# Kernel optimization log

Hardware: AMD Instinct MI355X
Metric: run time of the kernel (lower is better)

## Reference

```python
import jax, jax.numpy as jnp
import numpy as np

N = 16384
K = 16

def _w(k, shape):
    return jax.random.normal(k, shape, jnp.float32) * 0.05

def setup_inputs() -> dict:
    key = jax.random.key(0)
    ks = jax.random.split(key, 20)
    return {
        "img_feat": jax.random.normal(ks[0], (1, 32, N), jnp.float32),
        "cloud": jax.random.uniform(ks[1], (1, N, 3), jnp.float32),
        "conv1_w": _w(ks[2], (64, 32)),   "conv1_b": _w(ks[3], (64,)),
        "conv2_w": _w(ks[4], (128, 64)),  "conv2_b": _w(ks[5], (128,)),
        "psconv1_w": _w(ks[6], (256, 128)), "psconv1_b": _w(ks[7], (256,)),
        "psconv2_w": _w(ks[8], (128, 256)), "psconv2_b": _w(ks[9], (128,)),
        "pconv1_w": _w(ks[10], (64, 3)),  "pconv1_b": _w(ks[11], (64,)),
        "pconv2_w": _w(ks[12], (128, 64)),"pconv2_b": _w(ks[13], (128,)),
        "final_w": _w(ks[14], (32, 416)), "final_b": _w(ks[15], (32,)),
        "topk": K,
    }

def reference(img_feat, cloud, conv1_w, conv1_b, conv2_w, conv2_b,
              psconv1_w, psconv1_b, psconv2_w, psconv2_b,
              pconv1_w, pconv1_b, pconv2_w, pconv2_b,
              final_w, final_b, topk):
    lrelu = lambda x: jax.nn.leaky_relu(x, 0.01)
    pts = cloud[0]            # [N,3]  (module assumes bs=1)
    imf = img_feat[0].T       # [N,32]
    # point MLP: pconv1 -> lrelu -> pconv2 (Conv1d kernel=1 == per-point linear)
    cf = lrelu(pts @ pconv1_w.T + pconv1_b) @ pconv2_w.T + pconv2_b  # [N,128]
    # KNN: k smallest euclidean distances (self included)
    sq = jnp.sum(pts * pts, axis=-1)                 # [N]
    d2 = sq[:, None] + sq[None, :] - 2.0 * (pts @ pts.T)  # [N,N]
    _, idx = jax.lax.top_k(-d2, topk)                # [N,K]
    nb_pts = pts[idx]                                # [N,K,3]
    dist = jnp.sqrt(jnp.maximum(jnp.sum((pts[:, None, :] - nb_pts) ** 2, -1), 1e-12))
    wgt = jax.nn.softmax(-dist, axis=1)              # [N,K]
    nb_img = imf[idx]                                # [N,K,32]
    nb_cf = cf[idx]                                  # [N,K,128]
    sf = lrelu(nb_img @ conv1_w.T + conv1_b) @ conv2_w.T + conv2_b         # [N,K,128]
    sfp = lrelu(nb_cf @ psconv1_w.T + psconv1_b) @ psconv2_w.T + psconv2_b # [N,K,128]
    sf = jnp.max(sf * wgt[:, :, None], axis=1)       # weighted max-pool -> [N,128]
    sfp = jnp.max(sfp * wgt[:, :, None], axis=1)     # [N,128]
    final = jnp.concatenate([sfp, imf, sf, cf], axis=1)  # [N,416]
    out = lrelu(final) @ final_w.T + final_b         # [N,32]
    return out.T[None]                               # [1,32,N]
```

## Files before the change

kernel.cpp:

```cpp
#include <hip/hip_runtime.h>
#include <math.h>

#define N 16384
#define KNN 16
#define G 16
#define NCELL 4096

typedef __attribute__((ext_vector_type(8))) short bf16x8;
typedef __attribute__((ext_vector_type(4))) float f32x4;
typedef unsigned short ushort_t;
typedef unsigned long long u64;

__device__ __forceinline__ float lrelu(float a) { return a > 0.f ? a : 0.01f * a; }

__device__ __forceinline__ ushort_t f2bf(float f) {
  unsigned u = __float_as_uint(f);
  u += 0x7FFF + ((u >> 16) & 1);
  return (ushort_t)(u >> 16);
}
__device__ __forceinline__ float bf2f(ushort_t h) {
  return __uint_as_float((unsigned)h << 16);
}
__device__ __forceinline__ int lanerank(u64 mask) {
  return __builtin_amdgcn_mbcnt_hi((unsigned)(mask >> 32),
         __builtin_amdgcn_mbcnt_lo((unsigned)mask, 0));
}
__device__ __forceinline__ int cellof(float x) {
  int c = (int)(x * (float)G);
  return c < 0 ? 0 : (c > G - 1 ? G - 1 : c);
}

#define PPB 64
__global__ __launch_bounds__(256) void prepw_kernel(
    const float* __restrict__ img, const float* __restrict__ cloud,
    const float* __restrict__ p1w, const float* __restrict__ p1b,
    const float* __restrict__ p2w, const float* __restrict__ p2b,
    const float* __restrict__ ps1w, const float* __restrict__ ps2w,
    const float* __restrict__ c1w, const float* __restrict__ c2w,
    const float* __restrict__ fw,
    float4* __restrict__ pts4, ushort_t* __restrict__ cfh,
    ushort_t* __restrict__ imfh,
    ushort_t* __restrict__ w1h, ushort_t* __restrict__ w2h,
    ushort_t* __restrict__ c1h, ushort_t* __restrict__ c2h,
    float* __restrict__ fwp2, int* __restrict__ count) {
  int t = threadIdx.x;
  if (blockIdx.x >= 256) {
    int e = (blockIdx.x - 256) * 256 + t;
    if (e < 32768) w1h[e] = f2bf(ps1w[e]);
    else if (e < 65536) w2h[e - 32768] = f2bf(ps2w[e - 32768]);
    else if (e < 67584) c1h[e - 65536] = f2bf(c1w[e - 65536]);
    else if (e < 75776) c2h[e - 67584] = f2bf(c2w[e - 67584]);
    else if (e < 89088) {
      int e2 = e - 75776;
      int j4 = e2 >> 7, r2 = e2 & 127;
      int ch = r2 >> 2, sub = r2 & 3;
      fwp2[e2] = fw[ch * 416 + j4 * 4 + sub];
    }
    return;
  }
  __shared__ alignas(16) float w2t[64 * 132];
  __shared__ alignas(16) float hs[PPB * 68];
  __shared__ alignas(16) float w1s[192];
  __shared__ alignas(16) float b1s[64];
  __shared__ alignas(16) float b2s[128];
  __shared__ float ptmp[PPB * 3];
  __shared__ float psx[PPB], psy[PPB], psz[PPB];
  int pb = blockIdx.x * PPB;

  for (int e = t; e < 128 * 64; e += 256) {
    int ch = e >> 6, k = e & 63;
    w2t[k * 132 + ch] = p2w[e];
  }
  if (t < 192) w1s[t] = p1w[t];
  if (t < 64) b1s[t] = p1b[t];
  if (t < 128) b2s[t] = p2b[t];
  if (t < PPB * 3) ptmp[t] = cloud[pb * 3 + t];
  __syncthreads();
  if (t < PPB) {
    float x = ptmp[t * 3], y = ptmp[t * 3 + 1], z = ptmp[t * 3 + 2];
    psx[t] = x; psy[t] = y; psz[t] = z;
    pts4[pb + t] = make_float4(x, y, z, x * x + y * y + z * z);
    int cid = ((cellof(z) << 4) | cellof(y)) << 4 | cellof(x);
    atomicAdd(&count[cid], 1);
  }
  for (int e = t; e < 32 * PPB; e += 256) {
    int c = e >> 6, p = e & 63;
    imfh[(size_t)(pb + p) * 32 + c] = f2bf(img[(size_t)c * N + pb + p]);
  }
  __syncthreads();
  for (int e = t; e < PPB * 64; e += 256) {
    int pt_ = e >> 6, ch = e & 63;
    float a = b1s[ch] + psx[pt_] * w1s[ch * 3] + psy[pt_] * w1s[ch * 3 + 1] +
              psz[pt_] * w1s[ch * 3 + 2];
    hs[pt_ * 68 + ch] = lrelu(a);
  }
  __syncthreads();
  for (int e = t; e < PPB * 32; e += 256) {
    int pt_ = e >> 5, c4 = (e & 31) << 2;
    float4 acc = *(const float4*)&b2s[c4];
    const float* hrow = &hs[pt_ * 68];
    #pragma unroll
    for (int k = 0; k < 64; k += 4) {
      float4 h4 = *(const float4*)&hrow[k];
      float4 w0 = *(const float4*)&w2t[(k + 0) * 132 + c4];
      float4 w1_ = *(const float4*)&w2t[(k + 1) * 132 + c4];
      float4 w2_ = *(const float4*)&w2t[(k + 2) * 132 + c4];
      float4 w3 = *(const float4*)&w2t[(k + 3) * 132 + c4];
      acc.x = fmaf(h4.x, w0.x, fmaf(h4.y, w1_.x, fmaf(h4.z, w2_.x, fmaf(h4.w, w3.x, acc.x))));
      acc.y = fmaf(h4.x, w0.y, fmaf(h4.y, w1_.y, fmaf(h4.z, w2_.y, fmaf(h4.w, w3.y, acc.y))));
      acc.z = fmaf(h4.x, w0.z, fmaf(h4.y, w1_.z, fmaf(h4.z, w2_.z, fmaf(h4.w, w3.z, acc.z))));
      acc.w = fmaf(h4.x, w0.w, fmaf(h4.y, w1_.w, fmaf(h4.z, w2_.w, fmaf(h4.w, w3.w, acc.w))));
    }
    unsigned lo = (unsigned)f2bf(acc.x) | ((unsigned)f2bf(acc.y) << 16);
    unsigned hi = (unsigned)f2bf(acc.z) | ((unsigned)f2bf(acc.w) << 16);
    *(uint2*)&cfh[(size_t)(pb + pt_) * 128 + c4] = make_uint2(lo, hi);
  }
}

__global__ __launch_bounds__(256) void scan_kernel(
    const int* __restrict__ count, int* __restrict__ cellStart,
    int* __restrict__ cellofs) {
  __shared__ int part[256];
  int t = threadIdx.x;
  int local[16];
  int s = 0;
  #pragma unroll
  for (int j = 0; j < 16; ++j) { local[j] = s; s += count[t * 16 + j]; }
  part[t] = s;
  __syncthreads();
  for (int off = 1; off < 256; off <<= 1) {
    int v = (t >= off) ? part[t - off] : 0;
    __syncthreads();
    part[t] += v;
    __syncthreads();
  }
  int base = part[t] - s;
  #pragma unroll
  for (int j = 0; j < 16; ++j) {
    int v = base + local[j];
    cellStart[t * 16 + j] = v;
    cellofs[t * 16 + j] = v;
  }
  if (t == 255) cellStart[NCELL] = part[255];
}

__global__ __launch_bounds__(256) void scatter_kernel(
    const float4* __restrict__ pts4, const ushort_t* __restrict__ cfh,
    const ushort_t* __restrict__ imfh, int* __restrict__ cellofs,
    float4* __restrict__ spts, ushort_t* __restrict__ cfs,
    ushort_t* __restrict__ imfs) {
  __shared__ int sposl[256];
  int t = threadIdx.x;
  int pbase = blockIdx.x * 256;
  int p = pbase + t;
  float4 v = pts4[p];
  int cid = ((cellof(v.z) << 4) | cellof(v.y)) << 4 | cellof(v.x);
  int pos = atomicAdd(&cellofs[cid], 1);
  sposl[t] = pos;
  spts[pos] = make_float4(v.x, v.y, v.z, __int_as_float(p));
  __syncthreads();
  for (int e = t; e < 256 * 16; e += 256) {
    int row = e >> 4, part = e & 15;
    *(uint4*)&cfs[(size_t)sposl[row] * 128 + part * 8] =
        *(const uint4*)&cfh[(size_t)(pbase + row) * 128 + part * 8];
  }
  for (int e = t; e < 256 * 4; e += 256) {
    int row = e >> 2, part = e & 3;
    *(uint4*)&imfs[(size_t)sposl[row] * 32 + part * 8] =
        *(const uint4*)&imfh[(size_t)(pbase + row) * 32 + part * 8];
  }
}

#define NB_LD 136
#define S1_LD 264
#define NI_LD 40
#define H1_LD 72
__global__ __launch_bounds__(256) void ymlp_kernel(
    const ushort_t* __restrict__ cfs, const ushort_t* __restrict__ imfs,
    const ushort_t* __restrict__ w1h, const float* __restrict__ b1,
    const ushort_t* __restrict__ w2h, const float* __restrict__ b2,
    const ushort_t* __restrict__ c1h, const float* __restrict__ c1b,
    const ushort_t* __restrict__ c2h, const float* __restrict__ c2b,
    ushort_t* __restrict__ ycf, ushort_t* __restrict__ yimg) {
  __shared__ ushort_t nb[64 * NB_LD];
  __shared__ ushort_t s1[64 * S1_LD];
  int t = threadIdx.x;
  int w = t >> 6, lane = t & 63;
  int col = lane & 15, quad = lane >> 4;

  if (blockIdx.x < 256) {
    int pbase = blockIdx.x * 64;
    for (int e = t; e < 1024; e += 256) {
      int row = e >> 4, c8 = (e & 15) << 3;
      *(uint4*)&nb[row * NB_LD + c8] =
          *(const uint4*)&cfs[(size_t)(pbase + row) * 128 + c8];
    }
    __syncthreads();
    f32x4 acc1[4][4];
    #pragma unroll
    for (int tt = 0; tt < 4; ++tt)
      #pragma unroll
      for (int p = 0; p < 4; ++p) acc1[tt][p] = (f32x4){0.f, 0.f, 0.f, 0.f};
    for (int k0 = 0; k0 < 128; k0 += 32) {
      bf16x8 a[4];
      #pragma unroll
      for (int p = 0; p < 4; ++p)
        a[p] = *(const bf16x8*)&nb[(p * 16 + col) * NB_LD + k0 + quad * 8];
      #pragma unroll
      for (int tt = 0; tt < 4; ++tt) {
        int n = w * 64 + tt * 16 + col;
        bf16x8 b = *(const bf16x8*)&w1h[n * 128 + k0 + quad * 8];
        #pragma unroll
        for (int p = 0; p < 4; ++p)
          acc1[tt][p] = __builtin_amdgcn_mfma_f32_16x16x32_bf16(a[p], b, acc1[tt][p], 0, 0, 0);
      }
    }
    #pragma unroll
    for (int tt = 0; tt < 4; ++tt) {
      int n = w * 64 + tt * 16 + col;
      float bb = b1[n];
      #pragma unroll
      for (int p = 0; p < 4; ++p)
        #pragma unroll
        for (int r = 0; r < 4; ++r)
          s1[(p * 16 + quad * 4 + r) * S1_LD + n] = f2bf(lrelu(acc1[tt][p][r] + bb));
    }
    __syncthreads();
    f32x4 acc2[2][4];
    #pragma unroll
    for (int tt = 0; tt < 2; ++tt)
      #pragma unroll
      for (int p = 0; p < 4; ++p) acc2[tt][p] = (f32x4){0.f, 0.f, 0.f, 0.f};
    for (int k0 = 0; k0 < 256; k0 += 32) {
      bf16x8 a[4];
      #pragma unroll
      for (int p = 0; p < 4; ++p)
        a[p] = *(const bf16x8*)&s1[(p * 16 + col) * S1_LD + k0 + quad * 8];
      #pragma unroll
      for (int tt = 0; tt < 2; ++tt) {
        int n = w * 32 + tt * 16 + col;
        bf16x8 b = *(const bf16x8*)&w2h[n * 256 + k0 + quad * 8];
        #pragma unroll
        for (int p = 0; p < 4; ++p)
          acc2[tt][p] = __builtin_amdgcn_mfma_f32_16x16x32_bf16(a[p], b, acc2[tt][p], 0, 0, 0);
      }
    }
    #pragma unroll
    for (int tt = 0; tt < 2; ++tt) {
      int n = w * 32 + tt * 16 + col;
      float bb = b2[n];
      #pragma unroll
      for (int p = 0; p < 4; ++p)
        #pragma unroll
        for (int r = 0; r < 4; ++r)
          ycf[(size_t)(pbase + p * 16 + quad * 4 + r) * 128 + n] =
              f2bf(acc2[tt][p][r] + bb);
    }
  } else {
    int pbase = (blockIdx.x - 256) * 64;
    ushort_t* nbi = nb;
    ushort_t* h1 = s1;
    {
      int row = t >> 2, c8 = (t & 3) << 3;
      *(uint4*)&nbi[row * NI_LD + c8] =
          *(const uint4*)&imfs[(size_t)(pbase + row) * 32 + c8];
    }
    __syncthreads();
    {
      f32x4 accA[4];
      #pragma unroll
      for (int p = 0; p < 4; ++p) accA[p] = (f32x4){0.f, 0.f, 0.f, 0.f};
      int n = w * 16 + col;
      bf16x8 b = *(const bf16x8*)&c1h[n * 32 + quad * 8];
      #pragma unroll
      for (int p = 0; p < 4; ++p) {
        bf16x8 a = *(const bf16x8*)&nbi[(p * 16 + col) * NI_LD + quad * 8];
        accA[p] = __builtin_amdgcn_mfma_f32_16x16x32_bf16(a, b, accA[p], 0, 0, 0);
      }
      __syncthreads();
      float bb = c1b[n];
      #pragma unroll
      for (int p = 0; p < 4; ++p)
        #pragma unroll
        for (int r = 0; r < 4; ++r)
          h1[(p * 16 + quad * 4 + r) * H1_LD + n] = f2bf(lrelu(accA[p][r] + bb));
    }
    __syncthreads();
    f32x4 acc2[2][4];
    #pragma unroll
    for (int tt = 0; tt < 2; ++tt)
      #pragma unroll
      for (int p = 0; p < 4; ++p) acc2[tt][p] = (f32x4){0.f, 0.f, 0.f, 0.f};
    for (int k0 = 0; k0 < 64; k0 += 32) {
      bf16x8 a[4];
      #pragma unroll
      for (int p = 0; p < 4; ++p)
        a[p] = *(const bf16x8*)&h1[(p * 16 + col) * H1_LD + k0 + quad * 8];
      #pragma unroll
      for (int tt = 0; tt < 2; ++tt) {
        int n = w * 32 + tt * 16 + col;
        bf16x8 b = *(const bf16x8*)&c2h[n * 64 + k0 + quad * 8];
        #pragma unroll
        for (int p = 0; p < 4; ++p)
          acc2[tt][p] = __builtin_amdgcn_mfma_f32_16x16x32_bf16(a[p], b, acc2[tt][p], 0, 0, 0);
      }
    }
    #pragma unroll
    for (int tt = 0; tt < 2; ++tt) {
      int n = w * 32 + tt * 16 + col;
      float bb = c2b[n];
      #pragma unroll
      for (int p = 0; p < 4; ++p)
        #pragma unroll
        for (int r = 0; r < 4; ++r)
          yimg[(size_t)(pbase + p * 16 + quad * 4 + r) * 128 + n] =
              f2bf(acc2[tt][p][r] + bb);
    }
  }
}

__device__ __forceinline__ u64 bsort64(u64 v, int lane) {
  #pragma unroll
  for (int k = 2; k <= 64; k <<= 1) {
    #pragma unroll
    for (int j = k >> 1; j >= 1; j >>= 1) {
      u64 p = __shfl_xor(v, j);
      bool keepmin = (((lane & j) == 0) == ((lane & k) == 0));
      u64 mn = v < p ? v : p;
      u64 mx = v < p ? p : v;
      v = keepmin ? mn : mx;
    }
  }
  return v;
}

__device__ __forceinline__ u64 compact_topk(u64* buf, int& cnt, int lane, float& tau) {
  u64 v = (lane < cnt) ? buf[lane] : ~0ULL;
  v = bsort64(v, lane);
  if (cnt > 64) {
    u64 t = (64 + lane < cnt) ? buf[64 + lane] : ~0ULL;
    t = bsort64(t, lane);
    t = __shfl_xor(t, 63);
    v = (t < v) ? t : v;
    #pragma unroll
    for (int j = 32; j >= 1; j >>= 1) {
      u64 p = __shfl_xor(v, j);
      u64 mn = v < p ? v : p;
      u64 mx = v < p ? p : v;
      v = ((lane & j) == 0) ? mn : mx;
    }
  }
  if (lane < 16) buf[lane] = v;
  cnt = 16;
  u64 k15 = __shfl(v, 15);
  tau = __uint_as_float((unsigned)(k15 >> 28));
  if (!(tau == tau)) tau = INFINITY;
  return v;
}

__device__ __forceinline__ float tadj(float tau, float qw) {
  float a = tau - qw;
  return a + fabsf(a) * 2e-7f + 1e-35f;
}

__global__ __launch_bounds__(256) void knng_kernel(
    const float4* __restrict__ spts, const int* __restrict__ cellStart,
    const ushort_t* __restrict__ ycf, const ushort_t* __restrict__ yimg,
    const ushort_t* __restrict__ cfs, const ushort_t* __restrict__ imfs,
    const float* __restrict__ fwp2, const float* __restrict__ fb,
    float* __restrict__ out) {
  __shared__ u64 sbuf[4][128];
  __shared__ alignas(16) float feat[4][416];
  int t = threadIdx.x;
  int wv = t >> 6, lane = t & 63;
  int sb = (blockIdx.x & 7) * 512 + (blockIdx.x >> 3);
  int s = sb * 4 + wv;
  u64* buf = sbuf[wv];

  float4 q = spts[s];
  int oidq = __float_as_int(q.w);
  float qw = fmaf(q.z, q.z, fmaf(q.y, q.y, q.x * q.x));
  float q2x = -2.f * q.x, q2y = -2.f * q.y, q2z = -2.f * q.z;
  int cx = cellof(q.x), cy = cellof(q.y), cz = cellof(q.z);
  float tau = INFINITY;
  u64 vres;

  for (int r = 1;; ++r) {
    int lx = max(cx - r, 0), hx = min(cx + r, G - 1);
    int ly = max(cy - r, 0), hy = min(cy + r, G - 1);
    int lz = max(cz - r, 0), hz = min(cz + r, G - 1);
    int ny = hy - ly + 1, nz = hz - lz + 1, nruns = ny * nz;
    int cnt = 0;
    float ta = tadj(tau, qw);

    for (int rb = 0; rb < nruns; rb += 64) {
      int ln = rb + lane;
      int rs = 0, rc = 0;
      if (ln < nruns) {
        int z = lz + ln / ny, y = ly + ln % ny;
        int row = ((z << 4) | y) << 4;
        rs = cellStart[row + lx];
        rc = cellStart[row + hx + 1] - rs;
      }
      int off = rc;
      #pragma unroll
      for (int d = 1; d < 64; d <<= 1) {
        int v = __shfl_up(off, d);
        if (lane >= d) off += v;
      }
      int T = __shfl(off, 63);
      off -= rc;

      for (int cb = 0; cb < T; cb += 64) {
        int rk = cb + lane;
        int j = 0;
        #pragma unroll
        for (int step = 32; step; step >>= 1) {
          int nj = j + step;
          int onj = __shfl(off, nj & 63);
          if (nj < 64 && onj <= rk) j = nj;
        }
        int src = __shfl(rs, j) + rk - __shfl(off, j);
        bool valid = rk < T;
        if (!valid) src = 0;
        float4 c = spts[src];
        float cw = fmaf(c.z, c.z, fmaf(c.y, c.y, c.x * c.x));
        float d2 = fmaf(q2x, c.x, fmaf(q2y, c.y, fmaf(q2z, c.z, cw)));
        bool pass = valid && (d2 <= ta);
        u64 mask = __ballot(pass);
        if (mask) {
          if (pass) {
            unsigned oid = (unsigned)__float_as_int(c.w);
            u64 key = ((u64)__float_as_uint(fmaxf(d2 + qw, 0.f)) << 28) |
                      ((u64)oid << 14) | (unsigned)src;
            buf[cnt + lanerank(mask)] = key;
          }
          cnt += __popcll(mask);
          if (cnt > 64) {
            compact_topk(buf, cnt, lane, tau);
            ta = tadj(tau, qw);
          }
        }
      }
    }
    u64 v = compact_topk(buf, cnt, lane, tau);
    float cl = INFINITY;
    if (lx > 0)     cl = fminf(cl, q.x - (float)lx / (float)G);
    if (hx < G - 1) cl = fminf(cl, (float)(hx + 1) / (float)G - q.x);
    if (ly > 0)     cl = fminf(cl, q.y - (float)ly / (float)G);
    if (hy < G - 1) cl = fminf(cl, (float)(hy + 1) / (float)G - q.y);
    if (lz > 0)     cl = fminf(cl, q.z - (float)lz / (float)G);
    if (hz < G - 1) cl = fminf(cl, (float)(hz + 1) / (float)G - q.z);
    bool full = (lx == 0 && hx == G - 1 && ly == 0 && hy == G - 1 &&
                 lz == 0 && hz == G - 1);
    if (full || tau * 1.00002f <= cl * cl) { vres = v; break; }
  }

  int myspos = (lane < KNN) ? (int)(vres & 0x3FFF) : 0;
  float mywg = 0.f;
  {
    float4 c = spts[myspos];
    float dx = q.x - c.x, dy = q.y - c.y, dz = q.z - c.z;
    float dist = sqrtf(fmaxf(dx * dx + dy * dy + dz * dz, 1e-12f));
    float md = (lane < KNN) ? dist : INFINITY;
    #pragma unroll
    for (int off = 1; off < KNN; off <<= 1) md = fminf(md, __shfl_xor(md, off));
    float e = expf(md - dist);
    float se = (lane < KNN) ? e : 0.f;
    #pragma unroll
    for (int off = 1; off < KNN; off <<= 1) se += __shfl_xor(se, off);
    mywg = e / se;
  }

  int ksub = lane >> 4, c8 = lane & 15;
  float vimf = (lane < 32) ? bf2f(imfs[(size_t)s * 32 + lane]) : 0.f;
  unsigned vcf = *(const unsigned*)&cfs[(size_t)s * 128 + lane * 2];

  float a0[8], a1[8];
  #pragma unroll
  for (int j = 0; j < 8; ++j) { a0[j] = -INFINITY; a1[j] = -INFINITY; }
  #pragma unroll
  for (int kk = 0; kk < 4; ++kk) {
    int k = kk * 4 + ksub;
    int id = __shfl(myspos, k);
    float wg = __shfl(mywg, k);
    uint4 v = *(const uint4*)&ycf[(size_t)id * 128 + c8 * 8];
    uint4 u = *(const uint4*)&yimg[(size_t)id * 128 + c8 * 8];
    unsigned vv[4] = {v.x, v.y, v.z, v.w};
    unsigned uu[4] = {u.x, u.y, u.z, u.w};
    #pragma unroll
    for (int h = 0; h < 4; ++h) {
      a0[h * 2]     = fmaxf(a0[h * 2],     bf2f((ushort_t)(vv[h] & 0xffff)) * wg);
      a0[h * 2 + 1] = fmaxf(a0[h * 2 + 1], bf2f((ushort_t)(vv[h] >> 16)) * wg);
      a1[h * 2]     = fmaxf(a1[h * 2],     bf2f((ushort_t)(uu[h] & 0xffff)) * wg);
      a1[h * 2 + 1] = fmaxf(a1[h * 2 + 1], bf2f((ushort_t)(uu[h] >> 16)) * wg);
    }
  }
  #pragma unroll
  for (int j = 0; j < 8; ++j) {
    a0[j] = fmaxf(a0[j], __shfl_xor(a0[j], 16));
    a0[j] = fmaxf(a0[j], __shfl_xor(a0[j], 32));
    a1[j] = fmaxf(a1[j], __shfl_xor(a1[j], 16));
    a1[j] = fmaxf(a1[j], __shfl_xor(a1[j], 32));
  }
  if (lane < 16) {
    #pragma unroll
    for (int j = 0; j < 8; ++j) {
      feat[wv][c8 * 8 + j] = lrelu(a0[j]);
      feat[wv][160 + c8 * 8 + j] = lrelu(a1[j]);
    }
  }
  if (lane < 32) feat[wv][128 + lane] = lrelu(vimf);
  feat[wv][288 + lane * 2] = lrelu(bf2f((ushort_t)(vcf & 0xffff)));
  feat[wv][288 + lane * 2 + 1] = lrelu(bf2f((ushort_t)(vcf >> 16)));

  int ch = lane & 31, half = lane >> 5;
  float acc = half ? 0.f : fb[ch];
  const float* wr = fwp2 + (half * 52) * 128 + ch * 4;
  const float* fr = &feat[wv][half * 208];
  #pragma unroll 4
  for (int j4 = 0; j4 < 52; ++j4) {
    float4 w4 = *(const float4*)(wr + j4 * 128);
    float4 f4 = *(const float4*)(fr + j4 * 4);
    acc = fmaf(f4.x, w4.x, fmaf(f4.y, w4.y, fmaf(f4.z, w4.z, fmaf(f4.w, w4.w, acc))));
  }
  acc += __shfl_xor(acc, 32);
  if (lane < 32) out[(size_t)ch * N + oidq] = acc;
}

extern "C" void kernel_launch(void* const* d_in, const int* in_sizes, int n_in,
                              void* d_out, int out_size, void* d_ws, size_t ws_size,
                              hipStream_t stream) {
  const float* img   = (const float*)d_in[0];
  const float* cloud = (const float*)d_in[1];
  const float* c1w   = (const float*)d_in[2];
  const float* c1b   = (const float*)d_in[3];
  const float* c2w   = (const float*)d_in[4];
  const float* c2b   = (const float*)d_in[5];
  const float* ps1w  = (const float*)d_in[6];
  const float* ps1b  = (const float*)d_in[7];
  const float* ps2w  = (const float*)d_in[8];
  const float* ps2b  = (const float*)d_in[9];
  const float* p1w   = (const float*)d_in[10];
  const float* p1b   = (const float*)d_in[11];
  const float* p2w   = (const float*)d_in[12];
  const float* p2b   = (const float*)d_in[13];
  const float* fw    = (const float*)d_in[14];
  const float* fb    = (const float*)d_in[15];
  float* out = (float*)d_out;

  char* ws = (char*)d_ws;
  float4*   pts4  = (float4*)(ws + 0);
  ushort_t* cfh   = (ushort_t*)(ws + 262144);
  ushort_t* imfh  = (ushort_t*)(ws + 4456448);
  ushort_t* w1h   = (ushort_t*)(ws + 5505024);
  ushort_t* w2h   = (ushort_t*)(ws + 5570560);
  ushort_t* c1h   = (ushort_t*)(ws + 5636096);
  ushort_t* c2h   = (ushort_t*)(ws + 5640192);
  ushort_t* ycf   = (ushort_t*)(ws + 5656576);
  ushort_t* yimg  = (ushort_t*)(ws + 9850880);
  float4*   spts  = (float4*)(ws + 14045184);
  ushort_t* cfs   = (ushort_t*)(ws + 14307328);
  ushort_t* imfs  = (ushort_t*)(ws + 18501632);
  int*      cellStart = (int*)(ws + 19550208);
  int*      cellofs   = (int*)(ws + 19582976);
  int*      count     = (int*)(ws + 19599360);
  float*    fwp2      = (float*)(ws + 19615744);

  hipMemsetAsync(count, 0, NCELL * sizeof(int), stream);
  prepw_kernel<<<604, 256, 0, stream>>>(img, cloud, p1w, p1b, p2w, p2b,
                                        ps1w, ps2w, c1w, c2w, fw,
                                        pts4, cfh, imfh, w1h, w2h, c1h, c2h,
                                        fwp2, count);
  scan_kernel<<<1, 256, 0, stream>>>(count, cellStart, cellofs);
  scatter_kernel<<<64, 256, 0, stream>>>(pts4, cfh, imfh, cellofs,
                                         spts, cfs, imfs);
  ymlp_kernel<<<512, 256, 0, stream>>>(cfs, imfs, w1h, ps1b, w2h, ps2b,
                                       c1h, c1b, c2h, c2b, ycf, yimg);
  knng_kernel<<<N / 4, 256, 0, stream>>>(spts, cellStart, ycf, yimg,
                                         cfs, imfs, fwp2, fb, out);
}
```

Measured before the change: 192.3 us.

## Incremental shell KNN search with cell pruning and fused scan-scatter

The KNN search now keeps its candidate buffer across radius expansions and visits only cells of the new shell. Cells whose minimum box distance exceeds the current threshold are skipped, where before every cell in the cube was rescanned at each radius. Point norms are precomputed into the w component, with original ids moved to a separate array, and the buffer is enlarged so compaction runs less often. The single-block scan kernel is merged into the scatter kernel, with each block recomputing the prefix sum in shared memory. The risks are redundant scan work in every block and reliance on prepw supplying norms in pts4.w.

```diff
diff --git a/kernel.cpp b/kernel.cpp
--- a/kernel.cpp
+++ b/kernel.cpp
@@ -117,10 +117,15 @@
   }
 }
 
-__global__ __launch_bounds__(256) void scan_kernel(
-    const int* __restrict__ count, int* __restrict__ cellStart,
-    int* __restrict__ cellofs) {
+__global__ __launch_bounds__(256) void scatscan_kernel(
+    const float4* __restrict__ pts4, const ushort_t* __restrict__ cfh,
+    const ushort_t* __restrict__ imfh, const int* __restrict__ count,
+    int* __restrict__ count2, int* __restrict__ cellStartG,
+    float4* __restrict__ spts, int* __restrict__ soid,
+    ushort_t* __restrict__ cfs, ushort_t* __restrict__ imfs) {
+  __shared__ int cs[NCELL + 1];
   __shared__ int part[256];
+  __shared__ int sposl[256];
   int t = threadIdx.x;
   int local[16];
   int s = 0;
@@ -136,38 +141,33 @@
   }
   int base = part[t] - s;
   #pragma unroll
-  for (int j = 0; j < 16; ++j) {
-    int v = base + local[j];
-    cellStart[t * 16 + j] = v;
-    cellofs[t * 16 + j] = v;
-  }
-  if (t == 255) cellStart[NCELL] = part[255];
-}
-
-__global__ __launch_bounds__(256) void scatter_kernel(
-    const float4* __restrict__ pts4, const ushort_t* __restrict__ cfh,
-    const ushort_t* __restrict__ imfh, int* __restrict__ cellofs,
-    float4* __restrict__ spts, ushort_t* __restrict__ cfs,
-    ushort_t* __restrict__ imfs) {
-  __shared__ int sposl[256];
-  int t = threadIdx.x;
+  for (int j = 0; j < 16; ++j) cs[t * 16 + j] = base + local[j];
+  if (t == 255) cs[NCELL] = part[255];
+  if (blockIdx.x == 0) {
+    #pragma unroll
+    for (int j = 0; j < 16; ++j) cellStartG[t * 16 + j] = base + local[j];
+    if (t == 255) cellStartG[NCELL] = part[255];
+  }
+  __syncthreads();
+
   int pbase = blockIdx.x * 256;
   int p = pbase + t;
   float4 v = pts4[p];
   int cid = ((cellof(v.z) << 4) | cellof(v.y)) << 4 | cellof(v.x);
-  int pos = atomicAdd(&cellofs[cid], 1);
+  int pos = cs[cid] + atomicAdd(&count2[cid], 1);
   sposl[t] = pos;
-  spts[pos] = make_float4(v.x, v.y, v.z, __int_as_float(p));
+  spts[pos] = v;
+  soid[pos] = p;
   __syncthreads();
   for (int e = t; e < 256 * 16; e += 256) {
-    int row = e >> 4, part = e & 15;
-    *(uint4*)&cfs[(size_t)sposl[row] * 128 + part * 8] =
-        *(const uint4*)&cfh[(size_t)(pbase + row) * 128 + part * 8];
+    int row = e >> 4, part_ = e & 15;
+    *(uint4*)&cfs[(size_t)sposl[row] * 128 + part_ * 8] =
+        *(const uint4*)&cfh[(size_t)(pbase + row) * 128 + part_ * 8];
   }
   for (int e = t; e < 256 * 4; e += 256) {
-    int row = e >> 2, part = e & 3;
-    *(uint4*)&imfs[(size_t)sposl[row] * 32 + part * 8] =
-        *(const uint4*)&imfh[(size_t)(pbase + row) * 32 + part * 8];
+    int row = e >> 2, part_ = e & 3;
+    *(uint4*)&imfs[(size_t)sposl[row] * 32 + part_ * 8] =
+        *(const uint4*)&imfh[(size_t)(pbase + row) * 32 + part_ * 8];
   }
 }
 
@@ -337,8 +337,8 @@
 __device__ __forceinline__ u64 compact_topk(u64* buf, int& cnt, int lane, float& tau) {
   u64 v = (lane < cnt) ? buf[lane] : ~0ULL;
   v = bsort64(v, lane);
-  if (cnt > 64) {
-    u64 t = (64 + lane < cnt) ? buf[64 + lane] : ~0ULL;
+  for (int base = 64; base < cnt; base += 64) {
+    u64 t = (base + lane < cnt) ? buf[base + lane] : ~0ULL;
     t = bsort64(t, lane);
     t = __shfl_xor(t, 63);
     v = (t < v) ? t : v;
@@ -363,13 +363,15 @@
   return a + fabsf(a) * 2e-7f + 1e-35f;
 }
 
+#define BUFCAP 192
 __global__ __launch_bounds__(256) void knng_kernel(
-    const float4* __restrict__ spts, const int* __restrict__ cellStart,
+    const float4* __restrict__ spts, const int* __restrict__ soid,
+    const int* __restrict__ cellStart,
     const ushort_t* __restrict__ ycf, const ushort_t* __restrict__ yimg,
     const ushort_t* __restrict__ cfs, const ushort_t* __restrict__ imfs,
     const float* __restrict__ fwp2, const float* __restrict__ fb,
     float* __restrict__ out) {
-  __shared__ u64 sbuf[4][128];
+  __shared__ u64 sbuf[4][BUFCAP];
   __shared__ alignas(16) float feat[4][416];
   int t = threadIdx.x;
   int wv = t >> 6, lane = t & 63;
@@ -378,29 +380,46 @@
   u64* buf = sbuf[wv];
 
   float4 q = spts[s];
-  int oidq = __float_as_int(q.w);
-  float qw = fmaf(q.z, q.z, fmaf(q.y, q.y, q.x * q.x));
+  int oidq = soid[s];
+  float qw = q.w;
   float q2x = -2.f * q.x, q2y = -2.f * q.y, q2z = -2.f * q.z;
   int cx = cellof(q.x), cy = cellof(q.y), cz = cellof(q.z);
   float tau = INFINITY;
+  int cnt = 0;
+  int plx = 1, phx = 0, ply = 1, phy = 0, plz = 1, phz = 0;
   u64 vres;
+  const float invG = 1.f / (float)G;
 
   for (int r = 1;; ++r) {
     int lx = max(cx - r, 0), hx = min(cx + r, G - 1);
     int ly = max(cy - r, 0), hy = min(cy + r, G - 1);
     int lz = max(cz - r, 0), hz = min(cz + r, G - 1);
-    int ny = hy - ly + 1, nz = hz - lz + 1, nruns = ny * nz;
-    int cnt = 0;
+    int nx = hx - lx + 1, nyd = hy - ly + 1, nzd = hz - lz + 1;
+    int ncells = nx * nyd * nzd;
     float ta = tadj(tau, qw);
 
-    for (int rb = 0; rb < nruns; rb += 64) {
-      int ln = rb + lane;
+    for (int cb0 = 0; cb0 < ncells; cb0 += 64) {
+      int ci = cb0 + lane;
       int rs = 0, rc = 0;
-      if (ln < nruns) {
-        int z = lz + ln / ny, y = ly + ln % ny;
-        int row = ((z << 4) | y) << 4;
-        rs = cellStart[row + lx];
-        rc = cellStart[row + hx + 1] - rs;
+      if (ci < ncells) {
+        int x = lx + ci % nx;
+        int rem = ci / nx;
+        int y = ly + rem % nyd;
+        int z = lz + rem / nyd;
+        bool skip = (x >= plx && x <= phx && y >= ply && y <= phy &&
+                     z >= plz && z <= phz);
+        if (!skip) {
+          float bx0 = (float)x * invG, by0 = (float)y * invG, bz0 = (float)z * invG;
+          float dx = fmaxf(0.f, fmaxf(bx0 - q.x, q.x - (bx0 + invG)));
+          float dy = fmaxf(0.f, fmaxf(by0 - q.y, q.y - (by0 + invG)));
+          float dz = fmaxf(0.f, fmaxf(bz0 - q.z, q.z - (bz0 + invG)));
+          float mind2 = fmaf(dx, dx, fmaf(dy, dy, dz * dz));
+          if (!(mind2 - 1e-5f > tau)) {
+            int cid = ((z << 4) | y) << 4 | x;
+            rs = cellStart[cid];
+            rc = cellStart[cid + 1] - rs;
+          }
+        }
       }
       int off = rc;
       #pragma unroll
@@ -424,36 +443,33 @@
         bool valid = rk < T;
         if (!valid) src = 0;
         float4 c = spts[src];
-        float cw = fmaf(c.z, c.z, fmaf(c.y, c.y, c.x * c.x));
-        float d2 = fmaf(q2x, c.x, fmaf(q2y, c.y, fmaf(q2z, c.z, cw)));
+        int oid = soid[src];
+        float d2 = fmaf(q2x, c.x, fmaf(q2y, c.y, fmaf(q2z, c.z, c.w)));
         bool pass = valid && (d2 <= ta);
         u64 mask = __ballot(pass);
         if (mask) {
           if (pass) {
-            unsigned oid = (unsigned)__float_as_int(c.w);
             u64 key = ((u64)__float_as_uint(fmaxf(d2 + qw, 0.f)) << 28) |
-                      ((u64)oid << 14) | (unsigned)src;
+                      ((u64)(unsigned)oid << 14) | (unsigned)src;
             buf[cnt + lanerank(mask)] = key;
           }
           cnt += __popcll(mask);
-          if (cnt > 64) {
-            compact_topk(buf, cnt, lane, tau);
-            ta = tadj(tau, qw);
-          }
+          if (cnt > 128) { compact_topk(buf, cnt, lane, tau); ta = tadj(tau, qw); }
         }
       }
     }
     u64 v = compact_topk(buf, cnt, lane, tau);
     float cl = INFINITY;
-    if (lx > 0)     cl = fminf(cl, q.x - (float)lx / (float)G);
-    if (hx < G - 1) cl = fminf(cl, (float)(hx + 1) / (float)G - q.x);
-    if (ly > 0)     cl = fminf(cl, q.y - (float)ly / (float)G);
-    if (hy < G - 1) cl = fminf(cl, (float)(hy + 1) / (float)G - q.y);
-    if (lz > 0)     cl = fminf(cl, q.z - (float)lz / (float)G);
-    if (hz < G - 1) cl = fminf(cl, (float)(hz + 1) / (float)G - q.z);
+    if (lx > 0)     cl = fminf(cl, q.x - (float)lx * invG);
+    if (hx < G - 1) cl = fminf(cl, (float)(hx + 1) * invG - q.x);
+    if (ly > 0)     cl = fminf(cl, q.y - (float)ly * invG);
+    if (hy < G - 1) cl = fminf(cl, (float)(hy + 1) * invG - q.y);
+    if (lz > 0)     cl = fminf(cl, q.z - (float)lz * invG);
+    if (hz < G - 1) cl = fminf(cl, (float)(hz + 1) * invG - q.z);
     bool full = (lx == 0 && hx == G - 1 && ly == 0 && hy == G - 1 &&
                  lz == 0 && hz == G - 1);
     if (full || tau * 1.00002f <= cl * cl) { vres = v; break; }
+    plx = lx; phx = hx; ply = ly; phy = hy; plz = lz; phz = hz;
   }
 
   int myspos = (lane < KNN) ? (int)(vres & 0x3FFF) : 0;
@@ -563,20 +579,20 @@
   ushort_t* cfs   = (ushort_t*)(ws + 14307328);
   ushort_t* imfs  = (ushort_t*)(ws + 18501632);
   int*      cellStart = (int*)(ws + 19550208);
-  int*      cellofs   = (int*)(ws + 19582976);
-  int*      count     = (int*)(ws + 19599360);
+  int*      count     = (int*)(ws + 19582976);
+  int*      count2    = (int*)(ws + 19599360);
   float*    fwp2      = (float*)(ws + 19615744);
-
-  hipMemsetAsync(count, 0, NCELL * sizeof(int), stream);
+  int*      soid      = (int*)(ws + 19673088);
+
+  hipMemsetAsync(count, 0, 2 * NCELL * sizeof(int), stream);
   prepw_kernel<<<604, 256, 0, stream>>>(img, cloud, p1w, p1b, p2w, p2b,
                                         ps1w, ps2w, c1w, c2w, fw,
                                         pts4, cfh, imfh, w1h, w2h, c1h, c2h,
                                         fwp2, count);
-  scan_kernel<<<1, 256, 0, stream>>>(count, cellStart, cellofs);
-  scatter_kernel<<<64, 256, 0, stream>>>(pts4, cfh, imfh, cellofs,
-                                         spts, cfs, imfs);
+  scatscan_kernel<<<64, 256, 0, stream>>>(pts4, cfh, imfh, count, count2,
+                                          cellStart, spts, soid, cfs, imfs);
   ymlp_kernel<<<512, 256, 0, stream>>>(cfs, imfs, w1h, ps1b, w2h, ps2b,
                                        c1h, c1b, c2h, c2b, ycf, yimg);
-  knng_kernel<<<N / 4, 256, 0, stream>>>(spts, cellStart, ycf, yimg,
+  knng_kernel<<<N / 4, 256, 0, stream>>>(spts, soid, cellStart, ycf, yimg,
                                          cfs, imfs, fwp2, fb, out);
 }
```

After: 192.8 us. About the same (+0.3%).
